# Performance work log

Measured on AMD Instinct MI355X. Metric: run time of the kernel, lower is better.

The kernel has to match this reference:

```python
import jax, jax.numpy as jnp
import numpy as np

B, S, HID = 2, 2048, 2048
NH = 16
HD = HID // NH  # 128


def setup_inputs() -> dict:
    key = jax.random.key(0)
    ks = jax.random.split(key, 9)
    w = 0.02  # init scale to keep logits in a sane range
    return {
        "hidden_states": jax.random.normal(ks[0], (B, S, HID), dtype=jnp.float32),
        "Wq": jax.random.normal(ks[1], (HID, HID), dtype=jnp.float32) * w,
        "bq": jnp.zeros((HID,), dtype=jnp.float32),
        "Wk": jax.random.normal(ks[2], (HID, HD), dtype=jnp.float32) * w,
        "bk": jnp.zeros((HD,), dtype=jnp.float32),
        "Wv": jax.random.normal(ks[3], (HID, HD), dtype=jnp.float32) * w,
        "bv": jnp.zeros((HD,), dtype=jnp.float32),
        "Wo": jax.random.normal(ks[4], (HID, HID), dtype=jnp.float32) * w,
        "bo": jnp.zeros((HID,), dtype=jnp.float32),
    }


def reference(hidden_states, Wq, bq, Wk, bk, Wv, bv, Wo, bo):
    b, s, _ = hidden_states.shape
    # Projections (weights stored [in, out])
    q = hidden_states @ Wq + bq                      # [B,S,HID]
    k = hidden_states @ Wk + bk                      # [B,S,HD] single shared KV head
    v = hidden_states @ Wv + bv                      # [B,S,HD]
    q = q.reshape(b, s, NH, HD)                      # [B,S,H,D]
    # MQA: all query heads attend to the same K/V
    scores = jnp.einsum("bshd,btd->bhst", q, k) / jnp.sqrt(jnp.float32(HD))  # [B,H,S,S]
    probs = jax.nn.softmax(scores, axis=-1)
    attn = jnp.einsum("bhst,btd->bshd", probs, v)    # [B,S,H,D]
    attn = attn.reshape(b, s, HID)
    return attn @ Wo + bo
```

## Files before the change

kernel.cpp:

```cpp
#include <hip/hip_runtime.h>
#include <math.h>

#define BB  2
#define SS  2048
#define HID 2048
#define NH  16
#define HD  128
#define MT  (BB * SS)
#define NC  (HID + 2 * HD)
#define QK_SCALE 0.08838834764831845f

typedef unsigned short ushort_t;
typedef unsigned int uint_t;
typedef __bf16 bf16x8 __attribute__((ext_vector_type(8)));
typedef short short8 __attribute__((ext_vector_type(8)));
typedef float f32x4 __attribute__((ext_vector_type(4)));

__device__ __forceinline__ ushort_t f2bf(float x) {
    union { float f; uint_t u; } a; a.f = x;
    return (ushort_t)((a.u + 0x7FFFu + ((a.u >> 16) & 1u)) >> 16);
}
__device__ __forceinline__ ushort_t f2bf_fast(float x) {
    union { float f; uint_t u; } a; a.f = x;
    return (ushort_t)((a.u + 0x8000u) >> 16);
}

__device__ __forceinline__ int sw_addr(int r, int c) {
    return ((r >> 1) << 6) + ((((((r & 1) << 2) | c)) ^ ((r >> 1) & 7)) << 3);
}

#define CFENCE() asm volatile("" ::: "memory")

__global__ __launch_bounds__(256) void conv_bf16_kernel(
    const float* __restrict__ in, ushort_t* __restrict__ outb)
{
    const size_t i = ((size_t)blockIdx.x * 256 + threadIdx.x) * 8;
    const float4 a = *(const float4*)&in[i];
    const float4 b = *(const float4*)&in[i + 4];
    short8 o;
    o[0] = (short)f2bf(a.x); o[1] = (short)f2bf(a.y);
    o[2] = (short)f2bf(a.z); o[3] = (short)f2bf(a.w);
    o[4] = (short)f2bf(b.x); o[5] = (short)f2bf(b.y);
    o[6] = (short)f2bf(b.z); o[7] = (short)f2bf(b.w);
    *(short8*)&outb[i] = o;
}

__global__ __launch_bounds__(256) void convT_kernel(
    const float* __restrict__ W, ushort_t* __restrict__ Th, int K, int N)
{
    __shared__ float Ts[64][65];
    const int t = threadIdx.x;
    const int k0 = blockIdx.x * 64, n0 = blockIdx.y * 64;
    const int rr = t >> 4, c4 = (t & 15) * 4;
#pragma unroll
    for (int i = 0; i < 4; i++) {
        const int k = rr + i * 16;
        const float4 v = *(const float4*)&W[(size_t)(k0 + k) * N + n0 + c4];
        Ts[k][c4 + 0] = v.x; Ts[k][c4 + 1] = v.y;
        Ts[k][c4 + 2] = v.z; Ts[k][c4 + 3] = v.w;
    }
    __syncthreads();
    const int n = t >> 2, kc = (t & 3) * 16;
    short8 hv[2];
#pragma unroll
    for (int jj = 0; jj < 16; jj++)
        hv[jj >> 3][jj & 7] = (short)f2bf(Ts[kc + jj][n]);
    const size_t ob = (size_t)(n0 + n) * K + k0 + kc;
    *(short8*)&Th[ob]     = hv[0];
    *(short8*)&Th[ob + 8] = hv[1];
}

__global__ __launch_bounds__(256, 2) void gemm_qkv_kernel(
    const ushort_t* __restrict__ Ab, const ushort_t* __restrict__ WT,
    const float* __restrict__ bq, const float* __restrict__ bk,
    const float* __restrict__ bv,
    ushort_t* __restrict__ qb, ushort_t* __restrict__ kb,
    ushort_t* __restrict__ vtb)
{
    __shared__ short lds[8192];
    constexpr int AH = 0, BH = 4096;
    constexpr int K = HID;
    const int t  = threadIdx.x;
    const int wv = t >> 6, ln = t & 63;
    const int row0 = blockIdx.y * 128, col0 = blockIdx.x * 128;

    size_t agbase[2], bgbase[2];
    int    lbase[2];
#pragma unroll
    for (int i = 0; i < 2; i++) {
        const int I = wv * 2 + i;
        const int lrow = I * 8 + (ln >> 3);
        const int sb = (ln & 7) ^ (lrow & 7);
        const int rr = lrow * 2 + (sb >> 2);
        const int cc = sb & 3;
        agbase[i] = (size_t)(row0 + rr) * K + cc * 8;
        bgbase[i] = (size_t)(col0 + rr) * K + cc * 8;
        lbase[i] = I * 512;
    }

    const int wm0 = (wv & 1) * 64, wn0 = (wv >> 1) * 64;
    const int q = ln >> 4, lm = ln & 15;
    int aoff[4], boff[4];
#pragma unroll
    for (int i = 0; i < 4; i++) aoff[i] = sw_addr(wm0 + i * 16 + lm, q);
#pragma unroll
    for (int j = 0; j < 4; j++) boff[j] = sw_addr(wn0 + j * 16 + lm, q);

    f32x4 acc[4][4];
#pragma unroll
    for (int i = 0; i < 4; i++)
#pragma unroll
        for (int j = 0; j < 4; j++) acc[i][j] = 0.f;

    for (int k0 = 0; k0 < K; k0 += 32) {
        __syncthreads();
#pragma unroll
        for (int i = 0; i < 2; i++) {
            __builtin_amdgcn_global_load_lds(
                (const __attribute__((address_space(1))) void*)(Ab + agbase[i] + k0),
                (__attribute__((address_space(3))) void*)&lds[AH + lbase[i]], 16, 0, 0);
            __builtin_amdgcn_global_load_lds(
                (const __attribute__((address_space(1))) void*)(WT + bgbase[i] + k0),
                (__attribute__((address_space(3))) void*)&lds[BH + lbase[i]], 16, 0, 0);
        }
        __syncthreads();

        bf16x8 ah[4], bh[4];
#pragma unroll
        for (int i = 0; i < 4; i++) ah[i] = *(const bf16x8*)&lds[AH + aoff[i]];
#pragma unroll
        for (int j = 0; j < 4; j++) bh[j] = *(const bf16x8*)&lds[BH + boff[j]];
#pragma unroll
        for (int i = 0; i < 4; i++)
#pragma unroll
            for (int j = 0; j < 4; j++)
                acc[i][j] = __builtin_amdgcn_mfma_f32_16x16x32_bf16(ah[i], bh[j], acc[i][j], 0, 0, 0);
    }

    const int mode = (col0 < HID) ? 0 : ((col0 == HID) ? 1 : 2);
    const float* bsel = (mode == 0) ? bq : ((mode == 1) ? bk : bv);
    const int noff = (mode == 0) ? 0 : ((mode == 1) ? HID : HID + HD);
    float bj[4];
#pragma unroll
    for (int j = 0; j < 4; j++) bj[j] = bsel[col0 - noff + wn0 + j * 16 + lm];
#pragma unroll
    for (int i = 0; i < 4; i++) {
        const int mb = row0 + wm0 + i * 16 + q * 4;
#pragma unroll
        for (int j = 0; j < 4; j++) {
            const int nn = col0 + wn0 + j * 16 + lm;
#pragma unroll
            for (int rr2 = 0; rr2 < 4; rr2++) {
                const float v = acc[i][j][rr2] + bj[j];
                if (mode == 0)      qb [(size_t)(mb + rr2) * HID + nn]           = f2bf_fast(v * QK_SCALE);
                else if (mode == 1) kb [(size_t)(mb + rr2) * HD + (nn - HID)]    = f2bf_fast(v);
                else                vtb[(size_t)(nn - HID - HD) * MT + mb + rr2] = f2bf_fast(v);
            }
        }
    }
}

__global__ __launch_bounds__(256, 2) void gemm_oproj_kernel(
    const ushort_t* __restrict__ Ab, const ushort_t* __restrict__ WT,
    const float* __restrict__ bias, float* __restrict__ C, int M, int N, int K)
{
    __shared__ short lds[8192];
    constexpr int AH = 0, BH = 4096;
    const int t  = threadIdx.x;
    const int wv = t >> 6, ln = t & 63;
    const int row0 = blockIdx.y * 128, col0 = blockIdx.x * 128;

    size_t agbase[2], bgbase[2];
    int    lbase[2];
#pragma unroll
    for (int i = 0; i < 2; i++) {
        const int I = wv * 2 + i;
        const int lrow = I * 8 + (ln >> 3);
        const int sb = (ln & 7) ^ (lrow & 7);
        const int rr = lrow * 2 + (sb >> 2);
        const int cc = sb & 3;
        agbase[i] = (size_t)(row0 + rr) * K + cc * 8;
        bgbase[i] = (size_t)(col0 + rr) * K + cc * 8;
        lbase[i] = I * 512;
    }

    const int wm0 = (wv & 1) * 64, wn0 = (wv >> 1) * 64;
    const int q = ln >> 4, lm = ln & 15;
    int aoff[4], boff[4];
#pragma unroll
    for (int i = 0; i < 4; i++) aoff[i] = sw_addr(wm0 + i * 16 + lm, q);
#pragma unroll
    for (int j = 0; j < 4; j++) boff[j] = sw_addr(wn0 + j * 16 + lm, q);

    f32x4 acc[4][4];
#pragma unroll
    for (int i = 0; i < 4; i++)
#pragma unroll
        for (int j = 0; j < 4; j++) acc[i][j] = 0.f;

    for (int k0 = 0; k0 < K; k0 += 32) {
        __syncthreads();
#pragma unroll
        for (int i = 0; i < 2; i++) {
            __builtin_amdgcn_global_load_lds(
                (const __attribute__((address_space(1))) void*)(Ab + agbase[i] + k0),
                (__attribute__((address_space(3))) void*)&lds[AH + lbase[i]], 16, 0, 0);
            __builtin_amdgcn_global_load_lds(
                (const __attribute__((address_space(1))) void*)(WT + bgbase[i] + k0),
                (__attribute__((address_space(3))) void*)&lds[BH + lbase[i]], 16, 0, 0);
        }
        __syncthreads();

        bf16x8 ah[4], bh[4];
#pragma unroll
        for (int i = 0; i < 4; i++) ah[i] = *(const bf16x8*)&lds[AH + aoff[i]];
#pragma unroll
        for (int j = 0; j < 4; j++) bh[j] = *(const bf16x8*)&lds[BH + boff[j]];
#pragma unroll
        for (int i = 0; i < 4; i++)
#pragma unroll
            for (int j = 0; j < 4; j++)
                acc[i][j] = __builtin_amdgcn_mfma_f32_16x16x32_bf16(ah[i], bh[j], acc[i][j], 0, 0, 0);
    }

    float bj[4];
#pragma unroll
    for (int j = 0; j < 4; j++) bj[j] = bias[col0 + wn0 + j * 16 + lm];
#pragma unroll
    for (int i = 0; i < 4; i++) {
        const int mb = row0 + wm0 + i * 16 + q * 4;
#pragma unroll
        for (int j = 0; j < 4; j++) {
            const int nn = col0 + wn0 + j * 16 + lm;
#pragma unroll
            for (int rr2 = 0; rr2 < 4; rr2++)
                C[(size_t)(mb + rr2) * N + nn] = acc[i][j][rr2] + bj[j];
        }
    }
}

__global__ __launch_bounds__(128, 2) void attn_mfma_kernel(
    const ushort_t* __restrict__ qg, const ushort_t* __restrict__ kg,
    const ushort_t* __restrict__ vtg, ushort_t* Oh)
{
    __shared__ short Ks[8192], Vts[8192], Ps[4096];
    const int b = blockIdx.z, h = blockIdx.y, qt = blockIdx.x;
    const int t = threadIdx.x, wv = t >> 6, ln = t & 63;
    const int q = ln >> 4, lm = ln & 15;
    const int w32 = wv * 32;
    const int lm7 = ln & 7;

    const ushort_t* qgb = qg + (size_t)(b * SS + qt * 64) * HID + h * HD;
#pragma unroll
    for (int i = 0; i < 8; i++) {
        const int I = wv * 8 + i;
        const int r = 4 * I + (ln >> 4);
        const int c = (ln & 15) ^ (r & 15);
        __builtin_amdgcn_global_load_lds(
            (const __attribute__((address_space(1))) void*)(qgb + (size_t)r * HID + c * 8),
            (__attribute__((address_space(3))) void*)&Ks[I * 512], 16, 0, 0);
    }
    __syncthreads();
    bf16x8 aq[2][4];
#pragma unroll
    for (int st = 0; st < 2; st++) {
        const int am = w32 + st * 16 + lm;
#pragma unroll
        for (int ks = 0; ks < 4; ks++)
            aq[st][ks] = *(const bf16x8*)&Ks[am * 128 + (((ks << 2) | q) ^ (am & 15)) * 8];
    }
    __syncthreads();

    const ushort_t* kgb = kg + (size_t)b * SS * HD;
    const ushort_t* vgb = vtg + b * SS;
    uint_t koff[8], voff[8];
#pragma unroll
    for (int i = 0; i < 8; i++) {
        const int I = wv * 8 + i;
        { const int r = 4 * I + (ln >> 4); const int c = (ln & 15) ^ (r & 15);
          koff[i] = (uint_t)(r * HD + c * 8); }
        { const int r = 8 * I + (ln >> 3); const int c = (ln & 7) ^ (r & 7);
          voff[i] = (uint_t)(r * MT + c * 8); }
    }

#pragma unroll
    for (int i = 0; i < 8; i++) {
        const int I = wv * 8 + i;
        __builtin_amdgcn_global_load_lds(
            (const __attribute__((address_space(1))) void*)(kgb + koff[i]),
            (__attribute__((address_space(3))) void*)&Ks[I * 512], 16, 0, 0);
    }
#pragma unroll
    for (int i = 0; i < 8; i++) {
        const int I = wv * 8 + i;
        __builtin_amdgcn_global_load_lds(
            (const __attribute__((address_space(1))) void*)(vgb + voff[i]),
            (__attribute__((address_space(3))) void*)&Vts[I * 512], 16, 0, 0);
    }

    float lrow[2][4] = {{0.f, 0.f, 0.f, 0.f}, {0.f, 0.f, 0.f, 0.f}};
    f32x4 O[2][8];
#pragma unroll
    for (int st = 0; st < 2; st++)
#pragma unroll
        for (int ct = 0; ct < 8; ct++) O[st][ct] = 0.f;

    for (int kt = 0; kt < SS; kt += 64) {
        const int more = (kt + 64 < SS);

        asm volatile("s_waitcnt vmcnt(8)" ::: "memory");
        CFENCE();
        __builtin_amdgcn_s_barrier();
        CFENCE();

        f32x4 s[2][4];
#pragma unroll
        for (int st = 0; st < 2; st++)
#pragma unroll
            for (int ct = 0; ct < 4; ct++) s[st][ct] = 0.f;
        __builtin_amdgcn_s_setprio(1);
#pragma unroll
        for (int ks = 0; ks < 4; ks++) {
#pragma unroll
            for (int ct = 0; ct < 4; ct++) {
                const int n = ct * 16 + lm;
                const bf16x8 bk = *(const bf16x8*)&Ks[n * 128 + (((ks << 2) | q) ^ (n & 15)) * 8];
                s[0][ct] = __builtin_amdgcn_mfma_f32_16x16x32_bf16(aq[0][ks], bk, s[0][ct], 0, 0, 0);
                s[1][ct] = __builtin_amdgcn_mfma_f32_16x16x32_bf16(aq[1][ks], bk, s[1][ct], 0, 0, 0);
            }
        }
        __builtin_amdgcn_s_setprio(0);

        CFENCE();
        __builtin_amdgcn_s_barrier();
        CFENCE();
        if (more) {
#pragma unroll
            for (int i = 0; i < 8; i++) {
                const int I = wv * 8 + i;
                __builtin_amdgcn_global_load_lds(
                    (const __attribute__((address_space(1))) void*)(kgb + koff[i] + (kt + 64) * HD),
                    (__attribute__((address_space(3))) void*)&Ks[I * 512], 16, 0, 0);
            }
        }

#pragma unroll
        for (int st = 0; st < 2; st++)
#pragma unroll
        for (int ct = 0; ct < 4; ct++) {
            const int ch = ct * 2 + (lm >> 3);
#pragma unroll
            for (int r = 0; r < 4; r++) {
                const float p = __expf(s[st][ct][r]);
                lrow[st][r] += p;
                const int pr = w32 + st * 16 + q * 4 + r;
                Ps[pr * 64 + ((ch ^ (pr & 7)) << 3) + lm7] = (short)f2bf_fast(p);
            }
        }

        if (more) asm volatile("s_waitcnt vmcnt(8)" ::: "memory");
        else      asm volatile("s_waitcnt vmcnt(0)" ::: "memory");
        CFENCE();
        __builtin_amdgcn_s_barrier();
        CFENCE();

        __builtin_amdgcn_s_setprio(1);
#pragma unroll
        for (int ks = 0; ks < 2; ks++) {
            const bf16x8 ap0 = *(const bf16x8*)&Ps[(w32 + lm) * 64 + (((ks << 2) | q) ^ lm7) * 8];
            const bf16x8 ap1 = *(const bf16x8*)&Ps[(w32 + 16 + lm) * 64 + (((ks << 2) | q) ^ lm7) * 8];
#pragma unroll
            for (int ct = 0; ct < 8; ct++) {
                const int d = ct * 16 + lm;
                const bf16x8 bv = *(const bf16x8*)&Vts[d * 64 + (((ks << 2) | q) ^ (d & 7)) * 8];
                O[0][ct] = __builtin_amdgcn_mfma_f32_16x16x32_bf16(ap0, bv, O[0][ct], 0, 0, 0);
                O[1][ct] = __builtin_amdgcn_mfma_f32_16x16x32_bf16(ap1, bv, O[1][ct], 0, 0, 0);
            }
        }
        __builtin_amdgcn_s_setprio(0);

        CFENCE();
        __builtin_amdgcn_s_barrier();
        CFENCE();
        if (more) {
#pragma unroll
            for (int i = 0; i < 8; i++) {
                const int I = wv * 8 + i;
                __builtin_amdgcn_global_load_lds(
                    (const __attribute__((address_space(1))) void*)(vgb + voff[i] + (kt + 64)),
                    (__attribute__((address_space(3))) void*)&Vts[I * 512], 16, 0, 0);
            }
        }
    }

#pragma unroll
    for (int msk = 1; msk < 16; msk <<= 1)
#pragma unroll
        for (int st = 0; st < 2; st++)
#pragma unroll
            for (int r = 0; r < 4; r++) lrow[st][r] += __shfl_xor(lrow[st][r], msk);
#pragma unroll
    for (int st = 0; st < 2; st++)
#pragma unroll
    for (int r = 0; r < 4; r++) {
        const float inv = 1.f / lrow[st][r];
        const size_t base = (size_t)(b * SS + qt * 64 + w32 + st * 16 + q * 4 + r) * HID + h * HD;
#pragma unroll
        for (int ct = 0; ct < 8; ct++)
            Oh[base + ct * 16 + lm] = f2bf_fast(O[st][ct][r] * inv);
    }
}

extern "C" void kernel_launch(void* const* d_in, const int* in_sizes, int n_in,
                              void* d_out, int out_size, void* d_ws, size_t ws_size,
                              hipStream_t stream)
{
    const float* hs = (const float*)d_in[0];
    const float* Wq = (const float*)d_in[1];
    const float* bq = (const float*)d_in[2];
    const float* Wk = (const float*)d_in[3];
    const float* bk = (const float*)d_in[4];
    const float* Wv = (const float*)d_in[5];
    const float* bv = (const float*)d_in[6];
    const float* Wo = (const float*)d_in[7];
    const float* bo = (const float*)d_in[8];
    float* out = (float*)d_out;

    char* w = (char*)d_ws;
    ushort_t* hsb  = (ushort_t*)w;  w += (size_t)MT * HID * 2;
    ushort_t* qb   = (ushort_t*)w;  w += (size_t)MT * HID * 2;
    ushort_t* kb   = (ushort_t*)w;  w += (size_t)MT * HD * 2;
    ushort_t* vtb  = (ushort_t*)w;  w += (size_t)HD * MT * 2;
    ushort_t* WcT  = (ushort_t*)w;  w += (size_t)NC * HID * 2;
    ushort_t* WoT  = WcT;

    conv_bf16_kernel<<<(MT * HID) / (256 * 8), 256, 0, stream>>>(hs, hsb);
    convT_kernel<<<dim3(HID / 64, HID / 64), 256, 0, stream>>>(Wq, WcT, HID, HID);
    convT_kernel<<<dim3(HID / 64, HD / 64),  256, 0, stream>>>(
        Wk, WcT + (size_t)HID * HID, HID, HD);
    convT_kernel<<<dim3(HID / 64, HD / 64),  256, 0, stream>>>(
        Wv, WcT + (size_t)(HID + HD) * HID, HID, HD);

    gemm_qkv_kernel<<<dim3(NC / 128, MT / 128), 256, 0, stream>>>(
        hsb, WcT, bq, bk, bv, qb, kb, vtb);

    convT_kernel<<<dim3(HID / 64, HID / 64), 256, 0, stream>>>(Wo, WoT, HID, HID);

    attn_mfma_kernel<<<dim3(SS / 64, NH, BB), 128, 0, stream>>>(qb, kb, vtb, qb);

    gemm_oproj_kernel<<<dim3(HID / 128, MT / 128), 256, 0, stream>>>(
        qb, WoT, bo, out, MT, HID, HID);
}
```

Baseline: 322.0 us.

## Use 256x256 double-buffered GEMM tiles with block swizzle and exp2 softmax

Replaces the two 128x128 GEMM kernels (QKV projection and output projection) with one templated 256x256-tile kernel. It runs 512 threads, double-buffers LDS with async global-to-LDS prefetch of the next k-slice, raises wave priority around the MFMA loop, and remaps block IDs so consecutive blocks spread across XCDs. The aim is more data reuse per tile and overlap of loads with math. Separately, log2(e) is folded into the Q scale so the attention softmax can use exp2f instead of __expf. The cost is far fewer workgroups (144 and 128) than CUs, which risks leaving much of the GPU idle, and higher LDS and register use per block.

```diff
diff --git a/kernel.cpp b/kernel.cpp
--- a/kernel.cpp
+++ b/kernel.cpp
@@ -8,7 +8,7 @@
 #define HD  128
 #define MT  (BB * SS)
 #define NC  (HID + 2 * HD)
-#define QK_SCALE 0.08838834764831845f
+#define QK_SCALE 0.12751744f
 
 typedef unsigned short ushort_t;
 typedef unsigned int uint_t;
@@ -70,171 +70,131 @@
     *(short8*)&Th[ob + 8] = hv[1];
 }
 
-__global__ __launch_bounds__(256, 2) void gemm_qkv_kernel(
+template<int GX, int MODE>
+__global__ __launch_bounds__(512, 2) void gemm256_kernel(
     const ushort_t* __restrict__ Ab, const ushort_t* __restrict__ WT,
-    const float* __restrict__ bq, const float* __restrict__ bk,
-    const float* __restrict__ bv,
+    const float* __restrict__ bqp, const float* __restrict__ bkp,
+    const float* __restrict__ bvp,
     ushort_t* __restrict__ qb, ushort_t* __restrict__ kb,
-    ushort_t* __restrict__ vtb)
+    ushort_t* __restrict__ vtb, float* __restrict__ Cf)
 {
-    __shared__ short lds[8192];
-    constexpr int AH = 0, BH = 4096;
+    __shared__ short lds[32768];
     constexpr int K = HID;
-    const int t  = threadIdx.x;
-    const int wv = t >> 6, ln = t & 63;
-    const int row0 = blockIdx.y * 128, col0 = blockIdx.x * 128;
-
-    size_t agbase[2], bgbase[2];
-    int    lbase[2];
-#pragma unroll
-    for (int i = 0; i < 2; i++) {
-        const int I = wv * 2 + i;
-        const int lrow = I * 8 + (ln >> 3);
-        const int sb = (ln & 7) ^ (lrow & 7);
-        const int rr = lrow * 2 + (sb >> 2);
-        const int cc = sb & 3;
-        agbase[i] = (size_t)(row0 + rr) * K + cc * 8;
-        bgbase[i] = (size_t)(col0 + rr) * K + cc * 8;
-        lbase[i] = I * 512;
-    }
-
-    const int wm0 = (wv & 1) * 64, wn0 = (wv >> 1) * 64;
+    const int t = threadIdx.x;
+    const int w = t >> 6, ln = t & 63;
+    const int wm = w >> 2, wn = w & 3;
+    const int nh = wn >> 1;
     const int q = ln >> 4, lm = ln & 15;
-    int aoff[4], boff[4];
-#pragma unroll
-    for (int i = 0; i < 4; i++) aoff[i] = sw_addr(wm0 + i * 16 + lm, q);
-#pragma unroll
-    for (int j = 0; j < 4; j++) boff[j] = sw_addr(wn0 + j * 16 + lm, q);
-
-    f32x4 acc[4][4];
-#pragma unroll
-    for (int i = 0; i < 4; i++)
+
+    const int nwg = GX * (MT / 256);
+    const int bid = blockIdx.x;
+    const int sw = (bid & 7) * (nwg >> 3) + (bid >> 3);
+    const int bx = sw % GX, by = sw / GX;
+    const int row0 = by * 256, col0 = bx * 256;
+
+    const int lrow = w * 8 + (ln >> 3);
+    const int sb = (ln & 7) ^ (lrow & 7);
+    const int rs = lrow * 2 + (sb >> 2);
+    const int cc = sb & 3;
+    size_t agb[2], bgb[2];
+    agb[0] = (size_t)(row0 + rs) * K + cc * 8;
+    agb[1] = (size_t)(row0 + 128 + rs) * K + cc * 8;
+    bgb[0] = (size_t)(col0 + rs) * K + cc * 8;
+    bgb[1] = (size_t)(col0 + 128 + rs) * K + cc * 8;
+    const int lseg = w * 512;
+
+    int aofl[8], bofl[4];
+#pragma unroll
+    for (int mf = 0; mf < 8; mf++) aofl[mf] = sw_addr(mf * 16 + lm, q);
+#pragma unroll
+    for (int nf = 0; nf < 4; nf++) bofl[nf] = sw_addr((wn & 1) * 64 + nf * 16 + lm, q);
+
+#define ACH(bufv, hv) ((((bufv) << 1) | (hv)) << 12)
+#define STAGE_A(bufv, hv, kcol) \
+    __builtin_amdgcn_global_load_lds( \
+        (const __attribute__((address_space(1))) void*)(Ab + agb[hv] + (kcol)), \
+        (__attribute__((address_space(3))) void*)&lds[ACH(bufv, hv) + lseg], 16, 0, 0)
+#define STAGE_B(bufv, hv, kcol) \
+    __builtin_amdgcn_global_load_lds( \
+        (const __attribute__((address_space(1))) void*)(WT + bgb[hv] + (kcol)), \
+        (__attribute__((address_space(3))) void*)&lds[16384 + ACH(bufv, hv) + lseg], 16, 0, 0)
+
+    f32x4 acc[8][4];
+#pragma unroll
+    for (int i = 0; i < 8; i++)
 #pragma unroll
         for (int j = 0; j < 4; j++) acc[i][j] = 0.f;
 
-    for (int k0 = 0; k0 < K; k0 += 32) {
-        __syncthreads();
-#pragma unroll
-        for (int i = 0; i < 2; i++) {
-            __builtin_amdgcn_global_load_lds(
-                (const __attribute__((address_space(1))) void*)(Ab + agbase[i] + k0),
-                (__attribute__((address_space(3))) void*)&lds[AH + lbase[i]], 16, 0, 0);
-            __builtin_amdgcn_global_load_lds(
-                (const __attribute__((address_space(1))) void*)(WT + bgbase[i] + k0),
-                (__attribute__((address_space(3))) void*)&lds[BH + lbase[i]], 16, 0, 0);
-        }
-        __syncthreads();
-
-        bf16x8 ah[4], bh[4];
-#pragma unroll
-        for (int i = 0; i < 4; i++) ah[i] = *(const bf16x8*)&lds[AH + aoff[i]];
-#pragma unroll
-        for (int j = 0; j < 4; j++) bh[j] = *(const bf16x8*)&lds[BH + boff[j]];
-#pragma unroll
-        for (int i = 0; i < 4; i++)
-#pragma unroll
-            for (int j = 0; j < 4; j++)
-                acc[i][j] = __builtin_amdgcn_mfma_f32_16x16x32_bf16(ah[i], bh[j], acc[i][j], 0, 0, 0);
-    }
-
-    const int mode = (col0 < HID) ? 0 : ((col0 == HID) ? 1 : 2);
-    const float* bsel = (mode == 0) ? bq : ((mode == 1) ? bk : bv);
-    const int noff = (mode == 0) ? 0 : ((mode == 1) ? HID : HID + HD);
-    float bj[4];
-#pragma unroll
-    for (int j = 0; j < 4; j++) bj[j] = bsel[col0 - noff + wn0 + j * 16 + lm];
-#pragma unroll
-    for (int i = 0; i < 4; i++) {
-        const int mb = row0 + wm0 + i * 16 + q * 4;
-#pragma unroll
-        for (int j = 0; j < 4; j++) {
-            const int nn = col0 + wn0 + j * 16 + lm;
-#pragma unroll
-            for (int rr2 = 0; rr2 < 4; rr2++) {
-                const float v = acc[i][j][rr2] + bj[j];
-                if (mode == 0)      qb [(size_t)(mb + rr2) * HID + nn]           = f2bf_fast(v * QK_SCALE);
-                else if (mode == 1) kb [(size_t)(mb + rr2) * HD + (nn - HID)]    = f2bf_fast(v);
-                else                vtb[(size_t)(nn - HID - HD) * MT + mb + rr2] = f2bf_fast(v);
-            }
-        }
-    }
-}
-
-__global__ __launch_bounds__(256, 2) void gemm_oproj_kernel(
-    const ushort_t* __restrict__ Ab, const ushort_t* __restrict__ WT,
-    const float* __restrict__ bias, float* __restrict__ C, int M, int N, int K)
-{
-    __shared__ short lds[8192];
-    constexpr int AH = 0, BH = 4096;
-    const int t  = threadIdx.x;
-    const int wv = t >> 6, ln = t & 63;
-    const int row0 = blockIdx.y * 128, col0 = blockIdx.x * 128;
-
-    size_t agbase[2], bgbase[2];
-    int    lbase[2];
-#pragma unroll
-    for (int i = 0; i < 2; i++) {
-        const int I = wv * 2 + i;
-        const int lrow = I * 8 + (ln >> 3);
-        const int sb = (ln & 7) ^ (lrow & 7);
-        const int rr = lrow * 2 + (sb >> 2);
-        const int cc = sb & 3;
-        agbase[i] = (size_t)(row0 + rr) * K + cc * 8;
-        bgbase[i] = (size_t)(col0 + rr) * K + cc * 8;
-        lbase[i] = I * 512;
-    }
-
-    const int wm0 = (wv & 1) * 64, wn0 = (wv >> 1) * 64;
-    const int q = ln >> 4, lm = ln & 15;
-    int aoff[4], boff[4];
-#pragma unroll
-    for (int i = 0; i < 4; i++) aoff[i] = sw_addr(wm0 + i * 16 + lm, q);
-#pragma unroll
-    for (int j = 0; j < 4; j++) boff[j] = sw_addr(wn0 + j * 16 + lm, q);
-
-    f32x4 acc[4][4];
-#pragma unroll
-    for (int i = 0; i < 4; i++)
-#pragma unroll
-        for (int j = 0; j < 4; j++) acc[i][j] = 0.f;
-
-    for (int k0 = 0; k0 < K; k0 += 32) {
-        __syncthreads();
-#pragma unroll
-        for (int i = 0; i < 2; i++) {
-            __builtin_amdgcn_global_load_lds(
-                (const __attribute__((address_space(1))) void*)(Ab + agbase[i] + k0),
-                (__attribute__((address_space(3))) void*)&lds[AH + lbase[i]], 16, 0, 0);
-            __builtin_amdgcn_global_load_lds(
-                (const __attribute__((address_space(1))) void*)(WT + bgbase[i] + k0),
-                (__attribute__((address_space(3))) void*)&lds[BH + lbase[i]], 16, 0, 0);
-        }
-        __syncthreads();
-
-        bf16x8 ah[4], bh[4];
-#pragma unroll
-        for (int i = 0; i < 4; i++) ah[i] = *(const bf16x8*)&lds[AH + aoff[i]];
-#pragma unroll
-        for (int j = 0; j < 4; j++) bh[j] = *(const bf16x8*)&lds[BH + boff[j]];
-#pragma unroll
-        for (int i = 0; i < 4; i++)
-#pragma unroll
-            for (int j = 0; j < 4; j++)
-                acc[i][j] = __builtin_amdgcn_mfma_f32_16x16x32_bf16(ah[i], bh[j], acc[i][j], 0, 0, 0);
-    }
-
-    float bj[4];
-#pragma unroll
-    for (int j = 0; j < 4; j++) bj[j] = bias[col0 + wn0 + j * 16 + lm];
-#pragma unroll
-    for (int i = 0; i < 4; i++) {
-        const int mb = row0 + wm0 + i * 16 + q * 4;
-#pragma unroll
-        for (int j = 0; j < 4; j++) {
-            const int nn = col0 + wn0 + j * 16 + lm;
-#pragma unroll
-            for (int rr2 = 0; rr2 < 4; rr2++)
-                C[(size_t)(mb + rr2) * N + nn] = acc[i][j][rr2] + bj[j];
+    STAGE_A(0, 0, 0); STAGE_A(0, 1, 0);
+    STAGE_B(0, 0, 0); STAGE_B(0, 1, 0);
+
+    for (int kt = 0; kt < K; kt += 32) {
+        const int cur = (kt >> 5) & 1, nxt = cur ^ 1;
+        const bool more = (kt + 32 < K);
+
+        if (more) {
+            STAGE_A(nxt, 0, kt + 32); STAGE_A(nxt, 1, kt + 32);
+            STAGE_B(nxt, 0, kt + 32); STAGE_B(nxt, 1, kt + 32);
+            asm volatile("s_waitcnt vmcnt(4)" ::: "memory");
+        } else {
+            asm volatile("s_waitcnt vmcnt(0)" ::: "memory");
+        }
+        CFENCE(); __builtin_amdgcn_s_barrier(); CFENCE();
+
+        bf16x8 ah[8], bh[4];
+#pragma unroll
+        for (int mf = 0; mf < 8; mf++)
+            ah[mf] = *(const bf16x8*)&lds[ACH(cur, wm) + aofl[mf]];
+#pragma unroll
+        for (int nf = 0; nf < 4; nf++)
+            bh[nf] = *(const bf16x8*)&lds[16384 + ACH(cur, nh) + bofl[nf]];
+
+        __builtin_amdgcn_s_setprio(1);
+#pragma unroll
+        for (int mf = 0; mf < 8; mf++)
+#pragma unroll
+            for (int nf = 0; nf < 4; nf++)
+                acc[mf][nf] = __builtin_amdgcn_mfma_f32_16x16x32_bf16(
+                    ah[mf], bh[nf], acc[mf][nf], 0, 0, 0);
+        __builtin_amdgcn_s_setprio(0);
+
+        CFENCE(); __builtin_amdgcn_s_barrier(); CFENCE();
+    }
+#undef STAGE_A
+#undef STAGE_B
+#undef ACH
+
+#pragma unroll
+    for (int nf = 0; nf < 4; nf++) {
+        const int nnb = col0 + wn * 64 + nf * 16;
+        const int nn = nnb + lm;
+        if (MODE == 1) {
+            const float bj = bqp[nn];
+#pragma unroll
+            for (int mf = 0; mf < 8; mf++) {
+                const int mb = row0 + wm * 128 + mf * 16 + q * 4;
+#pragma unroll
+                for (int r = 0; r < 4; r++)
+                    Cf[(size_t)(mb + r) * HID + nn] = acc[mf][nf][r] + bj;
+            }
+        } else {
+            const int mode = (nnb < HID) ? 0 : ((nnb < HID + HD) ? 1 : 2);
+            const float bj = (mode == 0) ? bqp[nn]
+                           : (mode == 1) ? bkp[nn - HID] : bvp[nn - HID - HD];
+#pragma unroll
+            for (int mf = 0; mf < 8; mf++) {
+                const int mb = row0 + wm * 128 + mf * 16 + q * 4;
+#pragma unroll
+                for (int r = 0; r < 4; r++) {
+                    const float v = acc[mf][nf][r] + bj;
+                    if (mode == 0)
+                        qb[(size_t)(mb + r) * HID + nn] = f2bf_fast(v * QK_SCALE);
+                    else if (mode == 1)
+                        kb[(size_t)(mb + r) * HD + (nn - HID)] = f2bf_fast(v);
+                    else
+                        vtb[(size_t)(nn - HID - HD) * MT + (mb + r)] = f2bf_fast(v);
+                }
+            }
         }
     }
 }
@@ -351,7 +311,7 @@
             const int ch = ct * 2 + (lm >> 3);
 #pragma unroll
             for (int r = 0; r < 4; r++) {
-                const float p = __expf(s[st][ct][r]);
+                const float p = exp2f(s[st][ct][r]);
                 lrow[st][r] += p;
                 const int pr = w32 + st * 16 + q * 4 + r;
                 Ps[pr * 64 + ((ch ^ (pr & 7)) << 3) + lm7] = (short)f2bf_fast(p);
@@ -441,13 +401,13 @@
     convT_kernel<<<dim3(HID / 64, HD / 64),  256, 0, stream>>>(
         Wv, WcT + (size_t)(HID + HD) * HID, HID, HD);
 
-    gemm_qkv_kernel<<<dim3(NC / 128, MT / 128), 256, 0, stream>>>(
-        hsb, WcT, bq, bk, bv, qb, kb, vtb);
+    gemm256_kernel<NC / 256, 0><<<(NC / 256) * (MT / 256), 512, 0, stream>>>(
+        hsb, WcT, bq, bk, bv, qb, kb, vtb, nullptr);
 
     convT_kernel<<<dim3(HID / 64, HID / 64), 256, 0, stream>>>(Wo, WoT, HID, HID);
 
     attn_mfma_kernel<<<dim3(SS / 64, NH, BB), 128, 0, stream>>>(qb, kb, vtb, qb);
 
-    gemm_oproj_kernel<<<dim3(HID / 128, MT / 128), 256, 0, stream>>>(
-        qb, WoT, bo, out, MT, HID, HID);
-}
+    gemm256_kernel<HID / 256, 1><<<(HID / 256) * (MT / 256), 512, 0, stream>>>(
+        qb, WoT, bo, nullptr, nullptr, nullptr, nullptr, nullptr, out);
+}
```

New measurement: 359.5 us. 1.12x slower.
